# Performance work log

Measured on AMD Instinct MI355X. Metric: run time of the kernel, lower is better.

The kernel has to match this reference:

```python
import jax, jax.numpy as jnp
import numpy as np

EPS = 1e-12  # F.normalize eps
NUM_CLASSES = 80


def _l2_normalize(x, axis):
    # matches torch F.normalize: x / max(||x||_2, eps)
    n = jnp.sqrt(jnp.sum(x * x, axis=axis, keepdims=True))
    return x / jnp.maximum(n, EPS)


def setup_inputs() -> dict:
    key = jax.random.key(0)
    k1, k2, k3, k4 = jax.random.split(key, 4)
    B, C, H, W = 16, 256, 128, 128
    N = NUM_CLASSES
    features = jax.random.normal(k1, (B, C, H, W), dtype=jnp.float32)
    centroids = jax.random.normal(k2, (N, C), dtype=jnp.float32)
    fc_w = jax.random.normal(k3, (C, C, 1, 1), dtype=jnp.float32) * 0.02
    fc_b = jax.random.normal(k4, (C,), dtype=jnp.float32) * 0.01
    return {"features": features, "centroids": centroids, "fc_w": fc_w, "fc_b": fc_b}


def reference(features, centroids, fc_w, fc_b):
    N = centroids.shape[0]
    # cosine similarity to class centroids: [B, N, H, W]
    sim = jnp.einsum('bchw,nc->bnhw', _l2_normalize(features, axis=1),
                     _l2_normalize(centroids, axis=1))
    # hard one-hot assignment along class dim (scatter of argmax)
    idx = jnp.argmax(sim, axis=1)                              # [B, H, W]
    mask = jax.nn.one_hot(idx, N, axis=1, dtype=features.dtype)  # [B, N, H, W]
    # per-image, per-class mean feature (gather/blend)
    sum_x = jnp.einsum('bnhw,bchw->bnc', mask, features)       # [B, N, C]
    count = jnp.sum(mask, axis=(2, 3))[:, :, None]             # [B, N, 1]
    cent = sum_x / jnp.maximum(count, 1.0)
    delta = jnp.einsum('bnhw,bnc->bchw', mask, cent) - features
    alpha = jnp.exp(-jnp.mean(jnp.square(delta), axis=1, keepdims=True))  # [B,1,H,W]
    x = features + alpha * delta
    # 1x1 conv == channel matmul
    out = jnp.einsum('bchw,oc->bohw', x, fc_w[:, :, 0, 0]) + fc_b[None, :, None, None]
    return jax.nn.relu(out)
```

## Files before the change

kernel.cpp:

```cpp
#include <hip/hip_runtime.h>


typedef __bf16 bf16x8 __attribute__((ext_vector_type(8)));
typedef float  f32x4  __attribute__((ext_vector_type(4)));
typedef unsigned char u8;

__device__ __forceinline__ unsigned short f2b(float f) {
  unsigned u = __float_as_uint(f);
  return (unsigned short)((u + 0x7fffu + ((u >> 16) & 1u)) >> 16);
}
__device__ __forceinline__ float b2f(unsigned short s) {
  return __uint_as_float((unsigned)s << 16);
}

__global__ __launch_bounds__(256) void k0_cnorm(const float* __restrict__ cent,
                                                float* __restrict__ cnT,
                                                int* __restrict__ cntg) {
  int n = blockIdx.x, t = threadIdx.x;
  if (t < 16) cntg[n * 16 + t] = 0;
  float v = cent[n * 256 + t];
  float s = v * v;
  #pragma unroll
  for (int o = 32; o > 0; o >>= 1) s += __shfl_down(s, o, 64);
  __shared__ float red[4];
  if ((t & 63) == 0) red[t >> 6] = s;
  __syncthreads();
  float tot = red[0] + red[1] + red[2] + red[3];
  float dn = fmaxf(sqrtf(tot), 1e-12f);
  cnT[t * 80 + n] = v / dn;
}

__global__ __launch_bounds__(256) void k0_wprep(const float* __restrict__ fcw,
                                                unsigned short* __restrict__ wks,
                                                float* __restrict__ wt) {
  int o = blockIdx.x, c = threadIdx.x;
  float w = fcw[o * 256 + c];
  wt[c * 256 + o] = w;
  wks[((c >> 5) * 256 + o) * 32 + (c & 31)] = f2b(w);
}

__global__ __launch_bounds__(256) void k1_argmax(const float* __restrict__ feat,
                                                 const float* __restrict__ cnT,
                                                 u8* __restrict__ idxb,
                                                 float* __restrict__ fsqg,
                                                 int* __restrict__ cntg) {
  __shared__ int lh[80];
  int t = threadIdx.x;
  if (t < 80) lh[t] = 0;
  __syncthreads();
  int b = blockIdx.x >> 6;
  int pi = ((blockIdx.x & 63) << 8) | t;
  const float* fb = feat + (size_t)b * 256 * 16384 + pi;
  float g[80];
  #pragma unroll
  for (int n = 0; n < 80; ++n) g[n] = 0.f;
  float fsq = 0.f;
  #pragma unroll 4
  for (int c = 0; c < 256; ++c) {
    float v = fb[(size_t)c * 16384];
    fsq = fmaf(v, v, fsq);
    const float* cr = cnT + c * 80;
    #pragma unroll
    for (int n = 0; n < 80; ++n) g[n] = fmaf(v, cr[n], g[n]);
  }
  float best = g[0]; int bi = 0;
  #pragma unroll
  for (int n = 1; n < 80; ++n) if (g[n] > best) { best = g[n]; bi = n; }
  idxb[b * 16384 + pi] = (u8)bi;
  fsqg[b * 16384 + pi] = fsq;
  atomicAdd(&lh[bi], 1);
  __syncthreads();
  if (t < 80) atomicAdd(&cntg[b * 80 + t], lh[t]);
}

__global__ __launch_bounds__(256) void k1b_gemm(const float* __restrict__ feat,
                                                const u8* __restrict__ idxb,
                                                unsigned short* __restrict__ sumxp) {
  int bid = blockIdx.x;
  int kp = bid & 3, ns = (bid >> 2) & 7, b = bid >> 5;
  int t = threadIdx.x, wv = t >> 6, ln = t & 63, lo = ln & 15, hi = ln >> 4;
  int nt = wv & 1;
  int m0 = (wv >> 1) ? 3 : 0, nm = (wv >> 1) ? 2 : 3;
  int c = ns * 32 + nt * 16 + lo;
  const float* fp = feat + (((size_t)b * 256 + c) * 16384 + kp * 4096 + hi * 8);
  const u8* ip = idxb + b * 16384 + kp * 4096 + hi * 8;
  f32x4 acc[3];
  f32x4 zz = {0.f, 0.f, 0.f, 0.f};
  acc[0] = zz; acc[1] = zz; acc[2] = zz;
  for (int ks = 0; ks < 128; ++ks) {
    float4 v0 = *(const float4*)(fp + ks * 32);
    float4 v1 = *(const float4*)(fp + ks * 32 + 4);
    union { unsigned short u[8]; bf16x8 v; } bb;
    bb.u[0] = f2b(v0.x); bb.u[1] = f2b(v0.y); bb.u[2] = f2b(v0.z); bb.u[3] = f2b(v0.w);
    bb.u[4] = f2b(v1.x); bb.u[5] = f2b(v1.y); bb.u[6] = f2b(v1.z); bb.u[7] = f2b(v1.w);
    uint2 iv = *(const uint2*)(ip + ks * 32);
    int id[8];
    #pragma unroll
    for (int j = 0; j < 4; ++j) { id[j] = (iv.x >> (8 * j)) & 255; id[4 + j] = (iv.y >> (8 * j)) & 255; }
    #pragma unroll
    for (int mi = 0; mi < 3; ++mi) {
      if (mi >= nm) break;
      int row = (m0 + mi) * 16 + lo;
      union { unsigned short u[8]; bf16x8 v; } ma;
      #pragma unroll
      for (int j = 0; j < 8; ++j) ma.u[j] = (id[j] == row) ? (unsigned short)0x3F80 : (unsigned short)0;
      acc[mi] = __builtin_amdgcn_mfma_f32_16x16x32_bf16(ma.v, bb.v, acc[mi], 0, 0, 0);
    }
  }
  #pragma unroll
  for (int mi = 0; mi < 3; ++mi) {
    if (mi >= nm) break;
    #pragma unroll
    for (int r = 0; r < 4; ++r) {
      int cls = (m0 + mi) * 16 + hi * 4 + r;
      sumxp[(((size_t)kp * 16 + b) * 80 + cls) * 256 + ns * 32 + nt * 16 + lo] = f2b(acc[mi][r]);
    }
  }
}

__global__ __launch_bounds__(256) void k2_cent(const unsigned short* __restrict__ sumxp,
                                               const int* __restrict__ cntg,
                                               const float* __restrict__ wt,
                                               unsigned short* __restrict__ centf,
                                               float* __restrict__ csqg,
                                               float* __restrict__ chatg) {
  int bn = blockIdx.x; int t = threadIdx.x;
  float dn = fmaxf((float)cntg[bn], 1.0f);
  float s = 0.f;
  #pragma unroll
  for (int kp = 0; kp < 4; ++kp)
    s += b2f(sumxp[((size_t)kp * 1280 + bn) * 256 + t]);
  float cv = s / dn;
  __shared__ float cl[256];
  __shared__ float red[4];
  cl[t] = cv;
  centf[(size_t)bn * 256 + t] = f2b(cv);
  float q = cv * cv;
  #pragma unroll
  for (int o = 32; o > 0; o >>= 1) q += __shfl_down(q, o, 64);
  if ((t & 63) == 0) red[t >> 6] = q;
  __syncthreads();
  if (t == 0) csqg[bn] = red[0] + red[1] + red[2] + red[3];
  float acc = 0.f;
  #pragma unroll 4
  for (int c = 0; c < 256; ++c) acc = fmaf(wt[c * 256 + t], cl[c], acc);
  chatg[(size_t)bn * 256 + t] = acc;
}

__global__ __launch_bounds__(512) void k3b_gemm(const float* __restrict__ feat,
    const u8* __restrict__ idxb, const float* __restrict__ fsqg,
    const float* __restrict__ csqg, const unsigned short* __restrict__ centf,
    const float* __restrict__ chatg, const unsigned short* __restrict__ wks,
    const float* __restrict__ fcb, float* __restrict__ out) {
  __shared__ alignas(16) unsigned short featT[2][64 * 264];
  __shared__ float alphal[64];
  const int t = threadIdx.x;
  const int w = t >> 6, ln = t & 63, lo = ln & 15, hi = ln >> 4;
  const int pl = ln, cph = w;

  bf16x8 wf[2][8];
  #pragma unroll
  for (int ml = 0; ml < 2; ++ml)
    #pragma unroll
    for (int ks = 0; ks < 8; ++ks)
      wf[ml][ks] = *(const bf16x8*)&wks[((size_t)ks * 256 + (w * 2 + ml) * 16 + lo) * 32 + hi * 8];
  f32x4 bias2[2];
  #pragma unroll
  for (int ml = 0; ml < 2; ++ml)
    bias2[ml] = *(const f32x4*)&fcb[w * 32 + ml * 16 + hi * 4];

  const int tile0 = blockIdx.x * 8;
  {
    int b = tile0 >> 8, p0 = (tile0 & 255) << 6;
    const float* fb = feat + ((size_t)b * 256 + cph * 32) * 16384 + p0 + pl;
    #pragma unroll
    for (int jj = 0; jj < 4; ++jj) {
      union { unsigned short u[8]; uint4 q; } pk;
      #pragma unroll
      for (int e = 0; e < 8; ++e) pk.u[e] = f2b(fb[(size_t)(jj * 8 + e) * 16384]);
      *(uint4*)&featT[0][pl * 264 + cph * 32 + jj * 8] = pk.q;
    }
  }

  float nxv[32];
  for (int rep = 0; rep < 8; ++rep) {
    const int cur = rep & 1;
    const int tile = tile0 + rep;
    const int b = tile >> 8, p0 = (tile & 255) << 6;

    __syncthreads();

    if (rep < 7) {
      int t2 = tile + 1;
      int b2 = t2 >> 8, p02 = (t2 & 255) << 6;
      const float* fb2 = feat + ((size_t)b2 * 256 + cph * 32) * 16384 + p02 + pl;
      #pragma unroll
      for (int e = 0; e < 32; ++e) nxv[e] = fb2[(size_t)e * 16384];
    }

    {
      int p = t >> 3, sub = t & 7;
      int cid = idxb[b * 16384 + p0 + p];
      const unsigned short* cw = centf + ((size_t)b * 80 + cid) * 256 + sub * 32;
      const unsigned short* fr = &featT[cur][p * 264 + sub * 32];
      float sel = 0.f;
      #pragma unroll
      for (int j = 0; j < 4; ++j) {
        uint4 cc = *(const uint4*)&cw[j * 8];
        uint4 ff = *(const uint4*)&fr[j * 8];
        sel = fmaf(b2f((unsigned short)(ff.x & 0xffff)), b2f((unsigned short)(cc.x & 0xffff)), sel);
        sel = fmaf(b2f((unsigned short)(ff.x >> 16)),    b2f((unsigned short)(cc.x >> 16)),    sel);
        sel = fmaf(b2f((unsigned short)(ff.y & 0xffff)), b2f((unsigned short)(cc.y & 0xffff)), sel);
        sel = fmaf(b2f((unsigned short)(ff.y >> 16)),    b2f((unsigned short)(cc.y >> 16)),    sel);
        sel = fmaf(b2f((unsigned short)(ff.z & 0xffff)), b2f((unsigned short)(cc.z & 0xffff)), sel);
        sel = fmaf(b2f((unsigned short)(ff.z >> 16)),    b2f((unsigned short)(cc.z >> 16)),    sel);
        sel = fmaf(b2f((unsigned short)(ff.w & 0xffff)), b2f((unsigned short)(cc.w & 0xffff)), sel);
        sel = fmaf(b2f((unsigned short)(ff.w >> 16)),    b2f((unsigned short)(cc.w >> 16)),    sel);
      }
      sel += __shfl_xor(sel, 1, 64);
      sel += __shfl_xor(sel, 2, 64);
      sel += __shfl_xor(sel, 4, 64);
      if (sub == 0) {
        float fsq = fsqg[b * 16384 + p0 + p];
        float msq = (csqg[b * 80 + cid] - 2.f * sel + fsq) * (1.f / 256.f);
        alphal[p] = expf(-msq);
      }
    }

    f32x4 acc[2][4];
    f32x4 zz = {0.f, 0.f, 0.f, 0.f};
    #pragma unroll
    for (int ml = 0; ml < 2; ++ml)
      #pragma unroll
      for (int pt = 0; pt < 4; ++pt) acc[ml][pt] = zz;

    #pragma unroll
    for (int ks = 0; ks < 8; ++ks) {
      bf16x8 bfr[4];
      #pragma unroll
      for (int pt = 0; pt < 4; ++pt)
        bfr[pt] = *(const bf16x8*)&featT[cur][(pt * 16 + lo) * 264 + ks * 32 + hi * 8];
      #pragma unroll
      for (int ml = 0; ml < 2; ++ml)
        #pragma unroll
        for (int pt = 0; pt < 4; ++pt)
          acc[ml][pt] = __builtin_amdgcn_mfma_f32_16x16x32_bf16(wf[ml][ks], bfr[pt], acc[ml][pt], 0, 0, 0);
    }
    __syncthreads();

    #pragma unroll
    for (int pt = 0; pt < 4; ++pt) {
      int plx = pt * 16 + lo;
      int p = p0 + plx;
      float a = alphal[plx];
      float om = 1.f - a;
      int cid = idxb[b * 16384 + p];
      const float* crow = chatg + ((size_t)b * 80 + cid) * 256;
      #pragma unroll
      for (int ml = 0; ml < 2; ++ml) {
        int o0 = w * 32 + ml * 16 + hi * 4;
        float4 c4 = *(const float4*)&crow[o0];
        size_t ob = ((size_t)b * 256 + o0) * 16384 + p;
        out[ob            ] = fmaxf(fmaf(a, c4.x, om * acc[ml][pt][0]) + bias2[ml][0], 0.f);
        out[ob + 16384    ] = fmaxf(fmaf(a, c4.y, om * acc[ml][pt][1]) + bias2[ml][1], 0.f);
        out[ob + 2 * 16384] = fmaxf(fmaf(a, c4.z, om * acc[ml][pt][2]) + bias2[ml][2], 0.f);
        out[ob + 3 * 16384] = fmaxf(fmaf(a, c4.w, om * acc[ml][pt][3]) + bias2[ml][3], 0.f);
      }
    }

    if (rep < 7) {
      #pragma unroll
      for (int jj = 0; jj < 4; ++jj) {
        union { unsigned short u[8]; uint4 q; } pk;
        #pragma unroll
        for (int e = 0; e < 8; ++e) pk.u[e] = f2b(nxv[jj * 8 + e]);
        *(uint4*)&featT[cur ^ 1][pl * 264 + cph * 32 + jj * 8] = pk.q;
      }
    }
  }
}

extern "C" void kernel_launch(void* const* d_in, const int* in_sizes, int n_in,
                              void* d_out, int out_size, void* d_ws, size_t ws_size,
                              hipStream_t stream) {
  (void)in_sizes; (void)n_in; (void)out_size; (void)ws_size;
  const float* feat = (const float*)d_in[0];
  const float* cent = (const float*)d_in[1];
  const float* fcw  = (const float*)d_in[2];
  const float* fcb  = (const float*)d_in[3];
  float* out = (float*)d_out;
  char* ws = (char*)d_ws;
  float* cnT             = (float*)(ws);
  float* wt              = (float*)(ws + 81920);
  unsigned short* wks    = (unsigned short*)(ws + 344064);
  unsigned short* centf  = (unsigned short*)(ws + 475136);
  u8*    idxb            = (u8*)(ws + 1130496);
  float* fsq             = (float*)(ws + 1392640);
  int*   cntg            = (int*)(ws + 2441216);
  float* csq             = (float*)(ws + 2446336);
  float* chat            = (float*)(ws + 2451456);
  unsigned short* sumxp  = (unsigned short*)(ws + 3762176);

  k0_cnorm<<<80, 256, 0, stream>>>(cent, cnT, cntg);
  k0_wprep<<<256, 256, 0, stream>>>(fcw, wks, wt);
  k1_argmax<<<1024, 256, 0, stream>>>(feat, cnT, idxb, fsq, cntg);
  k1b_gemm<<<512, 256, 0, stream>>>(feat, idxb, sumxp);
  k2_cent<<<1280, 256, 0, stream>>>(sumxp, cntg, wt, centf, csq, chat);
  k3b_gemm<<<512, 512, 0, stream>>>(feat, idxb, fsq, csq, centf, chat, wks, fcb, out);
}
```

Measured before the change: 447.8 us.

## Emit bf16 feature copy in argmax pass and reuse it in later GEMMs

The argmax kernel now writes a bf16 copy of the features while it streams them, and both the class-sum GEMM and the final GEMM read this half-width copy instead of re-reading and converting the fp32 input. This lowers the total bytes moved for the two later passes and removes per-element conversions there. In exchange it adds a 128 MiB workspace write to the argmax pass, and k3b now does 16-bit strided loads that are packed into pairs.

```diff
diff --git a/kernel.cpp b/kernel.cpp
--- a/kernel.cpp
+++ b/kernel.cpp
@@ -43,7 +43,8 @@
                                                  const float* __restrict__ cnT,
                                                  u8* __restrict__ idxb,
                                                  float* __restrict__ fsqg,
-                                                 int* __restrict__ cntg) {
+                                                 int* __restrict__ cntg,
+                                                 unsigned short* __restrict__ featbf) {
   __shared__ int lh[80];
   int t = threadIdx.x;
   if (t < 80) lh[t] = 0;
@@ -51,6 +52,7 @@
   int b = blockIdx.x >> 6;
   int pi = ((blockIdx.x & 63) << 8) | t;
   const float* fb = feat + (size_t)b * 256 * 16384 + pi;
+  unsigned short* fo = featbf + (size_t)b * 256 * 16384 + pi;
   float g[80];
   #pragma unroll
   for (int n = 0; n < 80; ++n) g[n] = 0.f;
@@ -58,6 +60,7 @@
   #pragma unroll 4
   for (int c = 0; c < 256; ++c) {
     float v = fb[(size_t)c * 16384];
+    fo[(size_t)c * 16384] = f2b(v);
     fsq = fmaf(v, v, fsq);
     const float* cr = cnT + c * 80;
     #pragma unroll
@@ -73,7 +76,7 @@
   if (t < 80) atomicAdd(&cntg[b * 80 + t], lh[t]);
 }
 
-__global__ __launch_bounds__(256) void k1b_gemm(const float* __restrict__ feat,
+__global__ __launch_bounds__(256) void k1b_gemm(const unsigned short* __restrict__ featbf,
                                                 const u8* __restrict__ idxb,
                                                 unsigned short* __restrict__ sumxp) {
   int bid = blockIdx.x;
@@ -82,17 +85,13 @@
   int nt = wv & 1;
   int m0 = (wv >> 1) ? 3 : 0, nm = (wv >> 1) ? 2 : 3;
   int c = ns * 32 + nt * 16 + lo;
-  const float* fp = feat + (((size_t)b * 256 + c) * 16384 + kp * 4096 + hi * 8);
+  const unsigned short* fp = featbf + (((size_t)b * 256 + c) * 16384 + kp * 4096 + hi * 8);
   const u8* ip = idxb + b * 16384 + kp * 4096 + hi * 8;
   f32x4 acc[3];
   f32x4 zz = {0.f, 0.f, 0.f, 0.f};
   acc[0] = zz; acc[1] = zz; acc[2] = zz;
   for (int ks = 0; ks < 128; ++ks) {
-    float4 v0 = *(const float4*)(fp + ks * 32);
-    float4 v1 = *(const float4*)(fp + ks * 32 + 4);
-    union { unsigned short u[8]; bf16x8 v; } bb;
-    bb.u[0] = f2b(v0.x); bb.u[1] = f2b(v0.y); bb.u[2] = f2b(v0.z); bb.u[3] = f2b(v0.w);
-    bb.u[4] = f2b(v1.x); bb.u[5] = f2b(v1.y); bb.u[6] = f2b(v1.z); bb.u[7] = f2b(v1.w);
+    bf16x8 bv = *(const bf16x8*)(fp + ks * 32);
     uint2 iv = *(const uint2*)(ip + ks * 32);
     int id[8];
     #pragma unroll
@@ -104,7 +103,7 @@
       union { unsigned short u[8]; bf16x8 v; } ma;
       #pragma unroll
       for (int j = 0; j < 8; ++j) ma.u[j] = (id[j] == row) ? (unsigned short)0x3F80 : (unsigned short)0;
-      acc[mi] = __builtin_amdgcn_mfma_f32_16x16x32_bf16(ma.v, bb.v, acc[mi], 0, 0, 0);
+      acc[mi] = __builtin_amdgcn_mfma_f32_16x16x32_bf16(ma.v, bv, acc[mi], 0, 0, 0);
     }
   }
   #pragma unroll
@@ -147,7 +146,7 @@
   chatg[(size_t)bn * 256 + t] = acc;
 }
 
-__global__ __launch_bounds__(512) void k3b_gemm(const float* __restrict__ feat,
+__global__ __launch_bounds__(512) void k3b_gemm(const unsigned short* __restrict__ featbf,
     const u8* __restrict__ idxb, const float* __restrict__ fsqg,
     const float* __restrict__ csqg, const unsigned short* __restrict__ centf,
     const float* __restrict__ chatg, const unsigned short* __restrict__ wks,
@@ -172,17 +171,21 @@
   const int tile0 = blockIdx.x * 8;
   {
     int b = tile0 >> 8, p0 = (tile0 & 255) << 6;
-    const float* fb = feat + ((size_t)b * 256 + cph * 32) * 16384 + p0 + pl;
+    const unsigned short* fb = featbf + ((size_t)b * 256 + cph * 32) * 16384 + p0 + pl;
     #pragma unroll
     for (int jj = 0; jj < 4; ++jj) {
-      union { unsigned short u[8]; uint4 q; } pk;
-      #pragma unroll
-      for (int e = 0; e < 8; ++e) pk.u[e] = f2b(fb[(size_t)(jj * 8 + e) * 16384]);
-      *(uint4*)&featT[0][pl * 264 + cph * 32 + jj * 8] = pk.q;
-    }
-  }
-
-  float nxv[32];
+      unsigned pk[4];
+      #pragma unroll
+      for (int e = 0; e < 4; ++e) {
+        unsigned lo16 = fb[(size_t)(jj * 8 + 2 * e) * 16384];
+        unsigned hi16 = fb[(size_t)(jj * 8 + 2 * e + 1) * 16384];
+        pk[e] = lo16 | (hi16 << 16);
+      }
+      *(uint4*)&featT[0][pl * 264 + cph * 32 + jj * 8] = *(uint4*)pk;
+    }
+  }
+
+  unsigned nx[16];
   for (int rep = 0; rep < 8; ++rep) {
     const int cur = rep & 1;
     const int tile = tile0 + rep;
@@ -193,9 +196,13 @@
     if (rep < 7) {
       int t2 = tile + 1;
       int b2 = t2 >> 8, p02 = (t2 & 255) << 6;
-      const float* fb2 = feat + ((size_t)b2 * 256 + cph * 32) * 16384 + p02 + pl;
-      #pragma unroll
-      for (int e = 0; e < 32; ++e) nxv[e] = fb2[(size_t)e * 16384];
+      const unsigned short* fb2 = featbf + ((size_t)b2 * 256 + cph * 32) * 16384 + p02 + pl;
+      #pragma unroll
+      for (int e = 0; e < 16; ++e) {
+        unsigned lo16 = fb2[(size_t)(2 * e) * 16384];
+        unsigned hi16 = fb2[(size_t)(2 * e + 1) * 16384];
+        nx[e] = lo16 | (hi16 << 16);
+      }
     }
 
     {
@@ -270,12 +277,8 @@
 
     if (rep < 7) {
       #pragma unroll
-      for (int jj = 0; jj < 4; ++jj) {
-        union { unsigned short u[8]; uint4 q; } pk;
-        #pragma unroll
-        for (int e = 0; e < 8; ++e) pk.u[e] = f2b(nxv[jj * 8 + e]);
-        *(uint4*)&featT[cur ^ 1][pl * 264 + cph * 32 + jj * 8] = pk.q;
-      }
+      for (int jj = 0; jj < 4; ++jj)
+        *(uint4*)&featT[cur ^ 1][pl * 264 + cph * 32 + jj * 8] = *(uint4*)&nx[jj * 4];
     }
   }
 }
@@ -290,21 +293,22 @@
   const float* fcb  = (const float*)d_in[3];
   float* out = (float*)d_out;
   char* ws = (char*)d_ws;
-  float* cnT             = (float*)(ws);
-  float* wt              = (float*)(ws + 81920);
-  unsigned short* wks    = (unsigned short*)(ws + 344064);
-  unsigned short* centf  = (unsigned short*)(ws + 475136);
-  u8*    idxb            = (u8*)(ws + 1130496);
-  float* fsq             = (float*)(ws + 1392640);
-  int*   cntg            = (int*)(ws + 2441216);
-  float* csq             = (float*)(ws + 2446336);
-  float* chat            = (float*)(ws + 2451456);
-  unsigned short* sumxp  = (unsigned short*)(ws + 3762176);
+  unsigned short* featbf = (unsigned short*)(ws);
+  float* cnT             = (float*)(ws + 134217728);
+  float* wt              = (float*)(ws + 134299648);
+  unsigned short* wks    = (unsigned short*)(ws + 134561792);
+  unsigned short* centf  = (unsigned short*)(ws + 134692864);
+  u8*    idxb            = (u8*)(ws + 135348224);
+  float* fsq             = (float*)(ws + 135610368);
+  int*   cntg            = (int*)(ws + 136658944);
+  float* csq             = (float*)(ws + 136664064);
+  float* chat            = (float*)(ws + 136669184);
+  unsigned short* sumxp  = (unsigned short*)(ws + 137979904);
 
   k0_cnorm<<<80, 256, 0, stream>>>(cent, cnT, cntg);
   k0_wprep<<<256, 256, 0, stream>>>(fcw, wks, wt);
-  k1_argmax<<<1024, 256, 0, stream>>>(feat, cnT, idxb, fsq, cntg);
-  k1b_gemm<<<512, 256, 0, stream>>>(feat, idxb, sumxp);
+  k1_argmax<<<1024, 256, 0, stream>>>(feat, cnT, idxb, fsq, cntg, featbf);
+  k1b_gemm<<<512, 256, 0, stream>>>(featbf, idxb, sumxp);
   k2_cent<<<1280, 256, 0, stream>>>(sumxp, cntg, wt, centf, csq, chat);
-  k3b_gemm<<<512, 512, 0, stream>>>(feat, idxb, fsq, csq, centf, chat, wks, fcb, out);
-}
+  k3b_gemm<<<512, 512, 0, stream>>>(featbf, idxb, fsq, csq, centf, chat, wks, fcb, out);
+}
```

Result: slower. 505.2 us (+12.8%).
